# Optimization experiments

Measured on AMD Instinct MI355X. Metric: run time of the kernel, lower is better.

Reference implementation:

```python
import jax, jax.numpy as jnp
import numpy as np


def setup_inputs() -> dict:
    key = jax.random.key(0)
    k1, k2, k3 = jax.random.split(key, 3)
    B, N, C_IN, C_OUT = 8, 2048, 128, 64
    x = jax.random.normal(k1, (B, N, C_IN), dtype=jnp.float32)
    # Linear(c_in, c_out): weight [c_out, c_in], bias [c_out]
    W_adj = jax.random.normal(k2, (C_OUT, C_IN), dtype=jnp.float32) * (1.0 / np.sqrt(C_IN))
    b_adj = jax.random.normal(k3, (C_OUT,), dtype=jnp.float32) * 0.01
    return {"x": x, "W_adj": W_adj, "b_adj": b_adj}


def reference(x, W_adj, b_adj):
    # e_x = adj_projection(x): [B, N, C_out]
    e_x = jnp.einsum("bnc,oc->bno", x, W_adj) + b_adj
    # The original loop/concat builds all (i, j) pairs and takes per-pair
    # inner products; this is exactly the Gram matrix e_x @ e_x^T.
    lp = jax.nn.relu(jnp.tanh(jnp.einsum("bic,bjc->bij", e_x, e_x)))  # [B, N, N]
    num_neighbours = x.shape[1]
    node_feats = jnp.einsum("bij,bjc->bic", lp, e_x) / num_neighbours
    return node_feats, lp
```

## Files before the change

kernel.cpp:

```cpp
#include <hip/hip_runtime.h>
#include <hip/hip_bf16.h>


#define B_    8
#define N_    2048
#define D_    64
#define CIN_  128

typedef __bf16 bf16x8 __attribute__((ext_vector_type(8)));
typedef float f32x4  __attribute__((ext_vector_type(4)));

union FragU { uint4 u; bf16x8 f; };

static __device__ __forceinline__ bf16x8 ld_frag(const __hip_bfloat16* p) {
    FragU fu; fu.u = *reinterpret_cast<const uint4*>(p); return fu.f;
}

static __device__ __forceinline__ void st_frag(__hip_bfloat16* p, bf16x8 f) {
    FragU fu; fu.f = f; *reinterpret_cast<uint4*>(p) = fu.u;
}

static __device__ __forceinline__ void split8(const float* p, bf16x8& hi, bf16x8& lo) {
    const float4 a = *reinterpret_cast<const float4*>(p);
    const float4 b = *reinterpret_cast<const float4*>(p + 4);
    const float v[8] = {a.x, a.y, a.z, a.w, b.x, b.y, b.z, b.w};
#pragma unroll
    for (int i = 0; i < 8; i++) {
        const __bf16 h = (__bf16)v[i];
        hi[i] = h;
        lo[i] = (__bf16)(v[i] - (float)h);
    }
}

static __device__ __forceinline__ bf16x8 cvt8(const float* p) {
    const float4 a = *reinterpret_cast<const float4*>(p);
    const float4 b = *reinterpret_cast<const float4*>(p + 4);
    bf16x8 r;
    r[0] = (__bf16)a.x; r[1] = (__bf16)a.y; r[2] = (__bf16)a.z; r[3] = (__bf16)a.w;
    r[4] = (__bf16)b.x; r[5] = (__bf16)b.y; r[6] = (__bf16)b.z; r[7] = (__bf16)b.w;
    return r;
}

static __device__ __forceinline__ void lds_barrier() {
    asm volatile("s_waitcnt lgkmcnt(0)" ::: "memory");
    __builtin_amdgcn_s_barrier();
    __builtin_amdgcn_sched_barrier(0);
}

#define LDW  136

__global__ __launch_bounds__(256) void ex_kernel(
    const float* __restrict__ x,
    const float* __restrict__ W,
    const float* __restrict__ bias,
    __hip_bfloat16* __restrict__ e_hi,
    __hip_bfloat16* __restrict__ e_lo,
    __hip_bfloat16* __restrict__ e_hiT)
{
    __shared__ __align__(16) __hip_bfloat16 sW[2 * 64 * LDW];
    __hip_bfloat16* sWhi = sW;
    __hip_bfloat16* sWlo = sW + 64 * LDW;

    const int tid  = threadIdx.x;

#pragma unroll
    for (int p = 0; p < 4; p++) {
        const int q = tid + p * 256;
        const int r = q >> 4, c = (q & 15) * 8;
        bf16x8 hi, lo;
        split8(W + (size_t)r * CIN_ + c, hi, lo);
        st_frag(sWhi + r * LDW + c, hi);
        st_frag(sWlo + r * LDW + c, lo);
    }
    __syncthreads();

    const int w    = tid >> 6;
    const int lane = tid & 63;
    const int quad = lane >> 4;
    const int l16  = lane & 15;
    const int m0   = blockIdx.x * 64 + w * 16;

    const float* xrow = x + (size_t)(m0 + l16) * CIN_;
    bf16x8 ah[4], al[4];
#pragma unroll
    for (int ks = 0; ks < 4; ks++)
        split8(xrow + ks * 32 + quad * 8, ah[ks], al[ks]);

    f32x4 acc[4];
#pragma unroll
    for (int nt = 0; nt < 4; nt++) acc[nt] = f32x4{0.f, 0.f, 0.f, 0.f};

#pragma unroll
    for (int ks = 0; ks < 4; ks++) {
#pragma unroll
        for (int nt = 0; nt < 4; nt++) {
            bf16x8 wh = ld_frag(sWhi + (nt * 16 + l16) * LDW + ks * 32 + quad * 8);
            bf16x8 wl = ld_frag(sWlo + (nt * 16 + l16) * LDW + ks * 32 + quad * 8);
            acc[nt] = __builtin_amdgcn_mfma_f32_16x16x32_bf16(ah[ks], wh, acc[nt], 0, 0, 0);
            acc[nt] = __builtin_amdgcn_mfma_f32_16x16x32_bf16(ah[ks], wl, acc[nt], 0, 0, 0);
            acc[nt] = __builtin_amdgcn_mfma_f32_16x16x32_bf16(al[ks], wh, acc[nt], 0, 0, 0);
        }
    }

#pragma unroll
    for (int nt = 0; nt < 4; nt++) {
        const int chan = nt * 16 + l16;
        const float bv = bias[chan];
        union { __hip_bfloat16 h[4]; uint2 u2; } hv;
#pragma unroll
        for (int i = 0; i < 4; i++) {
            const int gr = m0 + quad * 4 + i;
            const float e = acc[nt][i] + bv;
            const __hip_bfloat16 hi = __float2bfloat16(e);
            const __hip_bfloat16 lo = __float2bfloat16(e - __bfloat162float(hi));
            e_hi[(size_t)gr * D_ + chan] = hi;
            e_lo[(size_t)gr * D_ + chan] = lo;
            hv.h[i] = hi;
        }
        const int gr0 = m0 + quad * 4;
        const int bt = gr0 >> 11, ir = gr0 & (N_ - 1);
        *reinterpret_cast<uint2*>(e_hiT + ((size_t)bt * D_ + chan) * N_ + ir) = hv.u2;
    }
}

#define LDE  72
#define LDT  136
#define LDF  132

__global__ __launch_bounds__(512, 4) void fused_kernel(
    const __hip_bfloat16* __restrict__ e_hi,
    const __hip_bfloat16* __restrict__ e_lo,
    const __hip_bfloat16* __restrict__ e_hiT,
    float* __restrict__ out)
{
    __shared__ __align__(16) unsigned char smem[32 * LDF * 4 + 128 * LDE * 2 * 2 + 64 * LDT * 2];
    float*          sLpF  = (float*)smem;
    __hip_bfloat16* sEhi  = (__hip_bfloat16*)(smem + 32 * LDF * 4);
    __hip_bfloat16* sElo  = sEhi + 128 * LDE;
    __hip_bfloat16* sEhiT = sElo + 128 * LDE;

    const int b   = blockIdx.x;
    const int i0  = blockIdx.y * 32;
    const int tid = threadIdx.x;
    const int w = tid >> 6, lane = tid & 63, quad = lane >> 4, l16 = lane & 15;
    const int g = w >> 2, h = w & 3;
    const int m0 = i0 + g * 16;
    const int koff = h * 32 + quad * 8;

    const int q2 = tid + 512;
    const int er1 = tid >> 3, ec1 = (tid & 7) * 8;
    const int er2 = q2  >> 3, ec2 = (q2  & 7) * 8;
    const int tr1 = tid >> 4, tc1 = (tid & 15) * 8;
    const int tr2 = q2  >> 4, tc2 = (q2  & 15) * 8;

    const __hip_bfloat16* eih = e_hi + (size_t)(b * N_ + m0 + l16) * D_;
    const __hip_bfloat16* eil = e_lo + (size_t)(b * N_ + m0 + l16) * D_;
    bf16x8 ahi[2], alo[2];
#pragma unroll
    for (int ks = 0; ks < 2; ks++) {
        ahi[ks] = ld_frag(eih + ks * 32 + quad * 8);
        alo[ks] = ld_frag(eil + ks * 32 + quad * 8);
    }

    f32x4 o[4];
#pragma unroll
    for (int nt = 0; nt < 4; nt++) o[nt] = f32x4{0.f, 0.f, 0.f, 0.f};

    float* lp_out = out + (size_t)B_ * N_ * D_;

    uint4 gh0, gh1, gl0, gl1, gt0, gt1;
    {
        gh0 = *(const uint4*)(e_hi + (size_t)(b * N_ + er1) * D_ + ec1);
        gh1 = *(const uint4*)(e_hi + (size_t)(b * N_ + er2) * D_ + ec2);
        gl0 = *(const uint4*)(e_lo + (size_t)(b * N_ + er1) * D_ + ec1);
        gl1 = *(const uint4*)(e_lo + (size_t)(b * N_ + er2) * D_ + ec2);
        gt0 = *(const uint4*)(e_hiT + (size_t)(b * D_ + tr1) * N_ + tc1);
        gt1 = *(const uint4*)(e_hiT + (size_t)(b * D_ + tr2) * N_ + tc2);
    }

    for (int jt = 0; jt < 16; jt++) {
        lds_barrier();

        if (jt > 0) {
            const int jc0 = (jt - 1) * 128;
#pragma unroll
            for (int p = 0; p < 2; p++) {
                const int q = tid + p * 512;
                const int r = q >> 5, c = (q & 31) * 4;
                __builtin_nontemporal_store(
                    *(const f32x4*)(sLpF + r * LDF + c),
                    (f32x4*)(lp_out + ((size_t)(b * N_ + i0 + r)) * N_ + jc0 + c));
            }
        }

        *(uint4*)(sEhi  + er1 * LDE + ec1) = gh0;
        *(uint4*)(sEhi  + er2 * LDE + ec2) = gh1;
        *(uint4*)(sElo  + er1 * LDE + ec1) = gl0;
        *(uint4*)(sElo  + er2 * LDE + ec2) = gl1;
        *(uint4*)(sEhiT + tr1 * LDT + tc1) = gt0;
        *(uint4*)(sEhiT + tr2 * LDT + tc2) = gt1;

        lds_barrier();

        {
            const int j0n = ((jt + 1) & 15) * 128;
            gh0 = *(const uint4*)(e_hi + (size_t)(b * N_ + j0n + er1) * D_ + ec1);
            gh1 = *(const uint4*)(e_hi + (size_t)(b * N_ + j0n + er2) * D_ + ec2);
            gl0 = *(const uint4*)(e_lo + (size_t)(b * N_ + j0n + er1) * D_ + ec1);
            gl1 = *(const uint4*)(e_lo + (size_t)(b * N_ + j0n + er2) * D_ + ec2);
            gt0 = *(const uint4*)(e_hiT + (size_t)(b * D_ + tr1) * N_ + j0n + tc1);
            gt1 = *(const uint4*)(e_hiT + (size_t)(b * D_ + tr2) * N_ + j0n + tc2);
        }

#pragma unroll
        for (int ntl = 0; ntl < 2; ntl++) {
            const int n0 = h * 32 + ntl * 16;
            f32x4 s = f32x4{0.f, 0.f, 0.f, 0.f};
#pragma unroll
            for (int ks = 0; ks < 2; ks++) {
                const int ko = ks * 32 + quad * 8;
                bf16x8 bhi = ld_frag(sEhi + (n0 + l16) * LDE + ko);
                bf16x8 blo = ld_frag(sElo + (n0 + l16) * LDE + ko);
                s = __builtin_amdgcn_mfma_f32_16x16x32_bf16(ahi[ks], bhi, s, 0, 0, 0);
                s = __builtin_amdgcn_mfma_f32_16x16x32_bf16(ahi[ks], blo, s, 0, 0, 0);
                s = __builtin_amdgcn_mfma_f32_16x16x32_bf16(alo[ks], bhi, s, 0, 0, 0);
            }
#pragma unroll
            for (int i = 0; i < 4; i++) {
                const float tc = fmaxf(s[i], 0.0f);
                const float z = __builtin_amdgcn_exp2f(tc * -2.8853900817779268f);
                const float v = (1.0f - z) * __builtin_amdgcn_rcpf(1.0f + z);
                sLpF[(g * 16 + quad * 4 + i) * LDF + n0 + l16] = v;
            }
        }

        {
            bf16x8 a = cvt8(sLpF + (g * 16 + l16) * LDF + koff);
#pragma unroll
            for (int nt = 0; nt < 4; nt++) {
                bf16x8 bfr = ld_frag(sEhiT + (nt * 16 + l16) * LDT + koff);
                o[nt] = __builtin_amdgcn_mfma_f32_16x16x32_bf16(a, bfr, o[nt], 0, 0, 0);
            }
        }
    }

    lds_barrier();
    {
        const int jc0 = 15 * 128;
#pragma unroll
        for (int p = 0; p < 2; p++) {
            const int q = tid + p * 512;
            const int r = q >> 5, c = (q & 31) * 4;
            __builtin_nontemporal_store(
                *(const f32x4*)(sLpF + r * LDF + c),
                (f32x4*)(lp_out + ((size_t)(b * N_ + i0 + r)) * N_ + jc0 + c));
        }
    }
    lds_barrier();

    float* sO = (float*)smem;
#pragma unroll
    for (int nt = 0; nt < 4; nt++) {
#pragma unroll
        for (int i = 0; i < 4; i++) {
            const int row = quad * 4 + i;
            const int chan = nt * 16 + l16;
            sO[w * 1088 + row * 68 + chan] = o[nt][i];
        }
    }
    lds_barrier();
    {
        const int row = tid >> 4;
        const int c4  = (tid & 15) * 4;
        const int gg = row >> 4, rr = row & 15;
        const float* base = sO + (gg * 4) * 1088 + rr * 68 + c4;
        const float4 v0 = *(const float4*)(base);
        const float4 v1 = *(const float4*)(base + 1088);
        const float4 v2 = *(const float4*)(base + 2176);
        const float4 v3 = *(const float4*)(base + 3264);
        f32x4 r;
        r[0] = (v0.x + v1.x + v2.x + v3.x) * (1.0f / 2048.0f);
        r[1] = (v0.y + v1.y + v2.y + v3.y) * (1.0f / 2048.0f);
        r[2] = (v0.z + v1.z + v2.z + v3.z) * (1.0f / 2048.0f);
        r[3] = (v0.w + v1.w + v2.w + v3.w) * (1.0f / 2048.0f);
        *reinterpret_cast<f32x4*>(out + ((size_t)(b * N_ + i0 + row)) * D_ + c4) = r;
    }
}

extern "C" void kernel_launch(void* const* d_in, const int* in_sizes, int n_in,
                              void* d_out, int out_size, void* d_ws, size_t ws_size,
                              hipStream_t stream) {
    const float* x    = (const float*)d_in[0];
    const float* W    = (const float*)d_in[1];
    const float* bias = (const float*)d_in[2];
    float* out = (float*)d_out;

    __hip_bfloat16* e_hi  = (__hip_bfloat16*)d_ws;
    __hip_bfloat16* e_lo  = e_hi + (size_t)B_ * N_ * D_;
    __hip_bfloat16* e_hiT = e_lo + (size_t)B_ * N_ * D_;

    ex_kernel<<<dim3(256), dim3(256), 0, stream>>>(x, W, bias, e_hi, e_lo, e_hiT);
    fused_kernel<<<dim3(8, 64), dim3(512), 0, stream>>>(e_hi, e_lo, e_hiT, out);
}
```

Baseline: 171.6 us.

## Merge projection and fused Gram kernels into one cooperative launch with grid sync

Folds the linear projection into the main kernel: each block computes its own 32-row slice of e_x (hi/lo split and transposed copy) into the workspace, then a cooperative grid-wide sync precedes the Gram/tanh/aggregation phase. This removes one kernel launch and the inter-kernel gap. In exchange it needs all 512 blocks co-resident, adds a grid barrier, and falls back to the two-kernel path if the cooperative launch fails.

```diff
diff --git a/kernel.cpp b/kernel.cpp
--- a/kernel.cpp
+++ b/kernel.cpp
@@ -1,5 +1,6 @@
 #include <hip/hip_runtime.h>
 #include <hip/hip_bf16.h>
+#include <hip/hip_cooperative_groups.h>
 
 
 #define B_    8
@@ -48,96 +49,20 @@
 }
 
 #define LDW  136
-
-__global__ __launch_bounds__(256) void ex_kernel(
+#define LDE  72
+#define LDT  136
+#define LDF  132
+
+__global__ __launch_bounds__(512, 4) void merged_kernel(
     const float* __restrict__ x,
     const float* __restrict__ W,
     const float* __restrict__ bias,
     __hip_bfloat16* __restrict__ e_hi,
     __hip_bfloat16* __restrict__ e_lo,
-    __hip_bfloat16* __restrict__ e_hiT)
-{
-    __shared__ __align__(16) __hip_bfloat16 sW[2 * 64 * LDW];
-    __hip_bfloat16* sWhi = sW;
-    __hip_bfloat16* sWlo = sW + 64 * LDW;
-
-    const int tid  = threadIdx.x;
-
-#pragma unroll
-    for (int p = 0; p < 4; p++) {
-        const int q = tid + p * 256;
-        const int r = q >> 4, c = (q & 15) * 8;
-        bf16x8 hi, lo;
-        split8(W + (size_t)r * CIN_ + c, hi, lo);
-        st_frag(sWhi + r * LDW + c, hi);
-        st_frag(sWlo + r * LDW + c, lo);
-    }
-    __syncthreads();
-
-    const int w    = tid >> 6;
-    const int lane = tid & 63;
-    const int quad = lane >> 4;
-    const int l16  = lane & 15;
-    const int m0   = blockIdx.x * 64 + w * 16;
-
-    const float* xrow = x + (size_t)(m0 + l16) * CIN_;
-    bf16x8 ah[4], al[4];
-#pragma unroll
-    for (int ks = 0; ks < 4; ks++)
-        split8(xrow + ks * 32 + quad * 8, ah[ks], al[ks]);
-
-    f32x4 acc[4];
-#pragma unroll
-    for (int nt = 0; nt < 4; nt++) acc[nt] = f32x4{0.f, 0.f, 0.f, 0.f};
-
-#pragma unroll
-    for (int ks = 0; ks < 4; ks++) {
-#pragma unroll
-        for (int nt = 0; nt < 4; nt++) {
-            bf16x8 wh = ld_frag(sWhi + (nt * 16 + l16) * LDW + ks * 32 + quad * 8);
-            bf16x8 wl = ld_frag(sWlo + (nt * 16 + l16) * LDW + ks * 32 + quad * 8);
-            acc[nt] = __builtin_amdgcn_mfma_f32_16x16x32_bf16(ah[ks], wh, acc[nt], 0, 0, 0);
-            acc[nt] = __builtin_amdgcn_mfma_f32_16x16x32_bf16(ah[ks], wl, acc[nt], 0, 0, 0);
-            acc[nt] = __builtin_amdgcn_mfma_f32_16x16x32_bf16(al[ks], wh, acc[nt], 0, 0, 0);
-        }
-    }
-
-#pragma unroll
-    for (int nt = 0; nt < 4; nt++) {
-        const int chan = nt * 16 + l16;
-        const float bv = bias[chan];
-        union { __hip_bfloat16 h[4]; uint2 u2; } hv;
-#pragma unroll
-        for (int i = 0; i < 4; i++) {
-            const int gr = m0 + quad * 4 + i;
-            const float e = acc[nt][i] + bv;
-            const __hip_bfloat16 hi = __float2bfloat16(e);
-            const __hip_bfloat16 lo = __float2bfloat16(e - __bfloat162float(hi));
-            e_hi[(size_t)gr * D_ + chan] = hi;
-            e_lo[(size_t)gr * D_ + chan] = lo;
-            hv.h[i] = hi;
-        }
-        const int gr0 = m0 + quad * 4;
-        const int bt = gr0 >> 11, ir = gr0 & (N_ - 1);
-        *reinterpret_cast<uint2*>(e_hiT + ((size_t)bt * D_ + chan) * N_ + ir) = hv.u2;
-    }
-}
-
-#define LDE  72
-#define LDT  136
-#define LDF  132
-
-__global__ __launch_bounds__(512, 4) void fused_kernel(
-    const __hip_bfloat16* __restrict__ e_hi,
-    const __hip_bfloat16* __restrict__ e_lo,
-    const __hip_bfloat16* __restrict__ e_hiT,
+    __hip_bfloat16* __restrict__ e_hiT,
     float* __restrict__ out)
 {
     __shared__ __align__(16) unsigned char smem[32 * LDF * 4 + 128 * LDE * 2 * 2 + 64 * LDT * 2];
-    float*          sLpF  = (float*)smem;
-    __hip_bfloat16* sEhi  = (__hip_bfloat16*)(smem + 32 * LDF * 4);
-    __hip_bfloat16* sElo  = sEhi + 128 * LDE;
-    __hip_bfloat16* sEhiT = sElo + 128 * LDE;
 
     const int b   = blockIdx.x;
     const int i0  = blockIdx.y * 32;
@@ -146,6 +71,63 @@
     const int g = w >> 2, h = w & 3;
     const int m0 = i0 + g * 16;
     const int koff = h * 32 + quad * 8;
+
+    {
+        __hip_bfloat16* sWhi = (__hip_bfloat16*)smem;
+        __hip_bfloat16* sWlo = sWhi + 64 * LDW;
+
+#pragma unroll
+        for (int p = 0; p < 2; p++) {
+            const int q = tid + p * 512;
+            const int r = q >> 4, c = (q & 15) * 8;
+            bf16x8 hi, lo;
+            split8(W + (size_t)r * CIN_ + c, hi, lo);
+            st_frag(sWhi + r * LDW + c, hi);
+            st_frag(sWlo + r * LDW + c, lo);
+        }
+        __syncthreads();
+
+        const float* xrow = x + (size_t)(b * N_ + m0 + l16) * CIN_;
+        bf16x8 ah[4], al[4];
+#pragma unroll
+        for (int ks = 0; ks < 4; ks++)
+            split8(xrow + ks * 32 + quad * 8, ah[ks], al[ks]);
+
+        const int chan = h * 16 + l16;
+        f32x4 acc = f32x4{0.f, 0.f, 0.f, 0.f};
+#pragma unroll
+        for (int ks = 0; ks < 4; ks++) {
+            bf16x8 wh = ld_frag(sWhi + chan * LDW + ks * 32 + quad * 8);
+            bf16x8 wl = ld_frag(sWlo + chan * LDW + ks * 32 + quad * 8);
+            acc = __builtin_amdgcn_mfma_f32_16x16x32_bf16(ah[ks], wh, acc, 0, 0, 0);
+            acc = __builtin_amdgcn_mfma_f32_16x16x32_bf16(ah[ks], wl, acc, 0, 0, 0);
+            acc = __builtin_amdgcn_mfma_f32_16x16x32_bf16(al[ks], wh, acc, 0, 0, 0);
+        }
+
+        const float bv = bias[chan];
+        union { __hip_bfloat16 hh[4]; uint2 u2; } hv;
+#pragma unroll
+        for (int i = 0; i < 4; i++) {
+            const int gr = b * N_ + m0 + quad * 4 + i;
+            const float e = acc[i] + bv;
+            const __hip_bfloat16 hi = __float2bfloat16(e);
+            const __hip_bfloat16 lo = __float2bfloat16(e - __bfloat162float(hi));
+            e_hi[(size_t)gr * D_ + chan] = hi;
+            e_lo[(size_t)gr * D_ + chan] = lo;
+            hv.hh[i] = hi;
+        }
+        const int ir = m0 + quad * 4;
+        *reinterpret_cast<uint2*>(e_hiT + ((size_t)(b * D_ + chan)) * N_ + ir) = hv.u2;
+        __syncthreads();
+    }
+
+    __threadfence();
+    cooperative_groups::this_grid().sync();
+
+    float*          sLpF  = (float*)smem;
+    __hip_bfloat16* sEhi  = (__hip_bfloat16*)(smem + 32 * LDF * 4);
+    __hip_bfloat16* sElo  = sEhi + 128 * LDE;
+    __hip_bfloat16* sEhiT = sElo + 128 * LDE;
 
     const int q2 = tid + 512;
     const int er1 = tid >> 3, ec1 = (tid & 7) * 8;
@@ -287,6 +269,239 @@
     }
 }
 
+__global__ __launch_bounds__(256) void ex_kernel(
+    const float* __restrict__ x,
+    const float* __restrict__ W,
+    const float* __restrict__ bias,
+    __hip_bfloat16* __restrict__ e_hi,
+    __hip_bfloat16* __restrict__ e_lo,
+    __hip_bfloat16* __restrict__ e_hiT)
+{
+    __shared__ __align__(16) __hip_bfloat16 sW[2 * 64 * LDW];
+    __hip_bfloat16* sWhi = sW;
+    __hip_bfloat16* sWlo = sW + 64 * LDW;
+
+    const int tid  = threadIdx.x;
+#pragma unroll
+    for (int p = 0; p < 4; p++) {
+        const int q = tid + p * 256;
+        const int r = q >> 4, c = (q & 15) * 8;
+        bf16x8 hi, lo;
+        split8(W + (size_t)r * CIN_ + c, hi, lo);
+        st_frag(sWhi + r * LDW + c, hi);
+        st_frag(sWlo + r * LDW + c, lo);
+    }
+    __syncthreads();
+
+    const int w    = tid >> 6;
+    const int lane = tid & 63;
+    const int quad = lane >> 4;
+    const int l16  = lane & 15;
+    const int m0   = blockIdx.x * 64 + w * 16;
+
+    const float* xrow = x + (size_t)(m0 + l16) * CIN_;
+    bf16x8 ah[4], al[4];
+#pragma unroll
+    for (int ks = 0; ks < 4; ks++)
+        split8(xrow + ks * 32 + quad * 8, ah[ks], al[ks]);
+
+    f32x4 acc[4];
+#pragma unroll
+    for (int nt = 0; nt < 4; nt++) acc[nt] = f32x4{0.f, 0.f, 0.f, 0.f};
+
+#pragma unroll
+    for (int ks = 0; ks < 4; ks++) {
+#pragma unroll
+        for (int nt = 0; nt < 4; nt++) {
+            bf16x8 wh = ld_frag(sWhi + (nt * 16 + l16) * LDW + ks * 32 + quad * 8);
+            bf16x8 wl = ld_frag(sWlo + (nt * 16 + l16) * LDW + ks * 32 + quad * 8);
+            acc[nt] = __builtin_amdgcn_mfma_f32_16x16x32_bf16(ah[ks], wh, acc[nt], 0, 0, 0);
+            acc[nt] = __builtin_amdgcn_mfma_f32_16x16x32_bf16(ah[ks], wl, acc[nt], 0, 0, 0);
+            acc[nt] = __builtin_amdgcn_mfma_f32_16x16x32_bf16(al[ks], wh, acc[nt], 0, 0, 0);
+        }
+    }
+
+#pragma unroll
+    for (int nt = 0; nt < 4; nt++) {
+        const int chan = nt * 16 + l16;
+        const float bv = bias[chan];
+        union { __hip_bfloat16 hh[4]; uint2 u2; } hv;
+#pragma unroll
+        for (int i = 0; i < 4; i++) {
+            const int gr = m0 + quad * 4 + i;
+            const float e = acc[nt][i] + bv;
+            const __hip_bfloat16 hi = __float2bfloat16(e);
+            const __hip_bfloat16 lo = __float2bfloat16(e - __bfloat162float(hi));
+            e_hi[(size_t)gr * D_ + chan] = hi;
+            e_lo[(size_t)gr * D_ + chan] = lo;
+            hv.hh[i] = hi;
+        }
+        const int gr0 = m0 + quad * 4;
+        const int bt = gr0 >> 11, ir = gr0 & (N_ - 1);
+        *reinterpret_cast<uint2*>(e_hiT + ((size_t)bt * D_ + chan) * N_ + ir) = hv.u2;
+    }
+}
+
+__global__ __launch_bounds__(512, 4) void fused_kernel(
+    const __hip_bfloat16* __restrict__ e_hi,
+    const __hip_bfloat16* __restrict__ e_lo,
+    const __hip_bfloat16* __restrict__ e_hiT,
+    float* __restrict__ out)
+{
+    __shared__ __align__(16) unsigned char smem[32 * LDF * 4 + 128 * LDE * 2 * 2 + 64 * LDT * 2];
+    float*          sLpF  = (float*)smem;
+    __hip_bfloat16* sEhi  = (__hip_bfloat16*)(smem + 32 * LDF * 4);
+    __hip_bfloat16* sElo  = sEhi + 128 * LDE;
+    __hip_bfloat16* sEhiT = sElo + 128 * LDE;
+
+    const int b   = blockIdx.x;
+    const int i0  = blockIdx.y * 32;
+    const int tid = threadIdx.x;
+    const int w = tid >> 6, lane = tid & 63, quad = lane >> 4, l16 = lane & 15;
+    const int g = w >> 2, h = w & 3;
+    const int m0 = i0 + g * 16;
+    const int koff = h * 32 + quad * 8;
+
+    const int q2 = tid + 512;
+    const int er1 = tid >> 3, ec1 = (tid & 7) * 8;
+    const int er2 = q2  >> 3, ec2 = (q2  & 7) * 8;
+    const int tr1 = tid >> 4, tc1 = (tid & 15) * 8;
+    const int tr2 = q2  >> 4, tc2 = (q2  & 15) * 8;
+
+    const __hip_bfloat16* eih = e_hi + (size_t)(b * N_ + m0 + l16) * D_;
+    const __hip_bfloat16* eil = e_lo + (size_t)(b * N_ + m0 + l16) * D_;
+    bf16x8 ahi[2], alo[2];
+#pragma unroll
+    for (int ks = 0; ks < 2; ks++) {
+        ahi[ks] = ld_frag(eih + ks * 32 + quad * 8);
+        alo[ks] = ld_frag(eil + ks * 32 + quad * 8);
+    }
+
+    f32x4 o[4];
+#pragma unroll
+    for (int nt = 0; nt < 4; nt++) o[nt] = f32x4{0.f, 0.f, 0.f, 0.f};
+
+    float* lp_out = out + (size_t)B_ * N_ * D_;
+
+    uint4 gh0, gh1, gl0, gl1, gt0, gt1;
+    {
+        gh0 = *(const uint4*)(e_hi + (size_t)(b * N_ + er1) * D_ + ec1);
+        gh1 = *(const uint4*)(e_hi + (size_t)(b * N_ + er2) * D_ + ec2);
+        gl0 = *(const uint4*)(e_lo + (size_t)(b * N_ + er1) * D_ + ec1);
+        gl1 = *(const uint4*)(e_lo + (size_t)(b * N_ + er2) * D_ + ec2);
+        gt0 = *(const uint4*)(e_hiT + (size_t)(b * D_ + tr1) * N_ + tc1);
+        gt1 = *(const uint4*)(e_hiT + (size_t)(b * D_ + tr2) * N_ + tc2);
+    }
+
+    for (int jt = 0; jt < 16; jt++) {
+        lds_barrier();
+
+        if (jt > 0) {
+            const int jc0 = (jt - 1) * 128;
+#pragma unroll
+            for (int p = 0; p < 2; p++) {
+                const int q = tid + p * 512;
+                const int r = q >> 5, c = (q & 31) * 4;
+                __builtin_nontemporal_store(
+                    *(const f32x4*)(sLpF + r * LDF + c),
+                    (f32x4*)(lp_out + ((size_t)(b * N_ + i0 + r)) * N_ + jc0 + c));
+            }
+        }
+
+        *(uint4*)(sEhi  + er1 * LDE + ec1) = gh0;
+        *(uint4*)(sEhi  + er2 * LDE + ec2) = gh1;
+        *(uint4*)(sElo  + er1 * LDE + ec1) = gl0;
+        *(uint4*)(sElo  + er2 * LDE + ec2) = gl1;
+        *(uint4*)(sEhiT + tr1 * LDT + tc1) = gt0;
+        *(uint4*)(sEhiT + tr2 * LDT + tc2) = gt1;
+
+        lds_barrier();
+
+        {
+            const int j0n = ((jt + 1) & 15) * 128;
+            gh0 = *(const uint4*)(e_hi + (size_t)(b * N_ + j0n + er1) * D_ + ec1);
+            gh1 = *(const uint4*)(e_hi + (size_t)(b * N_ + j0n + er2) * D_ + ec2);
+            gl0 = *(const uint4*)(e_lo + (size_t)(b * N_ + j0n + er1) * D_ + ec1);
+            gl1 = *(const uint4*)(e_lo + (size_t)(b * N_ + j0n + er2) * D_ + ec2);
+            gt0 = *(const uint4*)(e_hiT + (size_t)(b * D_ + tr1) * N_ + j0n + tc1);
+            gt1 = *(const uint4*)(e_hiT + (size_t)(b * D_ + tr2) * N_ + j0n + tc2);
+        }
+
+#pragma unroll
+        for (int ntl = 0; ntl < 2; ntl++) {
+            const int n0 = h * 32 + ntl * 16;
+            f32x4 s = f32x4{0.f, 0.f, 0.f, 0.f};
+#pragma unroll
+            for (int ks = 0; ks < 2; ks++) {
+                const int ko = ks * 32 + quad * 8;
+                bf16x8 bhi = ld_frag(sEhi + (n0 + l16) * LDE + ko);
+                bf16x8 blo = ld_frag(sElo + (n0 + l16) * LDE + ko);
+                s = __builtin_amdgcn_mfma_f32_16x16x32_bf16(ahi[ks], bhi, s, 0, 0, 0);
+                s = __builtin_amdgcn_mfma_f32_16x16x32_bf16(ahi[ks], blo, s, 0, 0, 0);
+                s = __builtin_amdgcn_mfma_f32_16x16x32_bf16(alo[ks], bhi, s, 0, 0, 0);
+            }
+#pragma unroll
+            for (int i = 0; i < 4; i++) {
+                const float tc = fmaxf(s[i], 0.0f);
+                const float z = __builtin_amdgcn_exp2f(tc * -2.8853900817779268f);
+                const float v = (1.0f - z) * __builtin_amdgcn_rcpf(1.0f + z);
+                sLpF[(g * 16 + quad * 4 + i) * LDF + n0 + l16] = v;
+            }
+        }
+
+        {
+            bf16x8 a = cvt8(sLpF + (g * 16 + l16) * LDF + koff);
+#pragma unroll
+            for (int nt = 0; nt < 4; nt++) {
+                bf16x8 bfr = ld_frag(sEhiT + (nt * 16 + l16) * LDT + koff);
+                o[nt] = __builtin_amdgcn_mfma_f32_16x16x32_bf16(a, bfr, o[nt], 0, 0, 0);
+            }
+        }
+    }
+
+    lds_barrier();
+    {
+        const int jc0 = 15 * 128;
+#pragma unroll
+        for (int p = 0; p < 2; p++) {
+            const int q = tid + p * 512;
+            const int r = q >> 5, c = (q & 31) * 4;
+            __builtin_nontemporal_store(
+                *(const f32x4*)(sLpF + r * LDF + c),
+                (f32x4*)(lp_out + ((size_t)(b * N_ + i0 + r)) * N_ + jc0 + c));
+        }
+    }
+    lds_barrier();
+
+    float* sO = (float*)smem;
+#pragma unroll
+    for (int nt = 0; nt < 4; nt++) {
+#pragma unroll
+        for (int i = 0; i < 4; i++) {
+            const int row = quad * 4 + i;
+            const int chan = nt * 16 + l16;
+            sO[w * 1088 + row * 68 + chan] = o[nt][i];
+        }
+    }
+    lds_barrier();
+    {
+        const int row = tid >> 4;
+        const int c4  = (tid & 15) * 4;
+        const int gg = row >> 4, rr = row & 15;
+        const float* base = sO + (gg * 4) * 1088 + rr * 68 + c4;
+        const float4 v0 = *(const float4*)(base);
+        const float4 v1 = *(const float4*)(base + 1088);
+        const float4 v2 = *(const float4*)(base + 2176);
+        const float4 v3 = *(const float4*)(base + 3264);
+        f32x4 r;
+        r[0] = (v0.x + v1.x + v2.x + v3.x) * (1.0f / 2048.0f);
+        r[1] = (v0.y + v1.y + v2.y + v3.y) * (1.0f / 2048.0f);
+        r[2] = (v0.z + v1.z + v2.z + v3.z) * (1.0f / 2048.0f);
+        r[3] = (v0.w + v1.w + v2.w + v3.w) * (1.0f / 2048.0f);
+        *reinterpret_cast<f32x4*>(out + ((size_t)(b * N_ + i0 + row)) * D_ + c4) = r;
+    }
+}
+
 extern "C" void kernel_launch(void* const* d_in, const int* in_sizes, int n_in,
                               void* d_out, int out_size, void* d_ws, size_t ws_size,
                               hipStream_t stream) {
@@ -299,6 +514,13 @@
     __hip_bfloat16* e_lo  = e_hi + (size_t)B_ * N_ * D_;
     __hip_bfloat16* e_hiT = e_lo + (size_t)B_ * N_ * D_;
 
-    ex_kernel<<<dim3(256), dim3(256), 0, stream>>>(x, W, bias, e_hi, e_lo, e_hiT);
-    fused_kernel<<<dim3(8, 64), dim3(512), 0, stream>>>(e_hi, e_lo, e_hiT, out);
-}
+    void* args[] = {(void*)&x, (void*)&W, (void*)&bias,
+                    (void*)&e_hi, (void*)&e_lo, (void*)&e_hiT, (void*)&out};
+    hipError_t err = hipLaunchCooperativeKernel(
+        reinterpret_cast<const void*>(merged_kernel),
+        dim3(8, 64), dim3(512), args, 0, stream);
+    if (err != hipSuccess) {
+        ex_kernel<<<dim3(256), dim3(256), 0, stream>>>(x, W, bias, e_hi, e_lo, e_hiT);
+        fused_kernel<<<dim3(8, 64), dim3(512), 0, stream>>>(e_hi, e_lo, e_hiT, out);
+    }
+}
```

After: 317.7 us. 1.85x slower.
